# Kernel optimization log

Measured on AMD Instinct MI355X. Metric: run time of the kernel, lower is better.

## Reference

```python
import jax, jax.numpy as jnp
import numpy as np

B, N, E = 32, 256, 300   # batch, num hyperedges, word emb size
H, K = 256, 8            # nhidden, nhead
MARGIN = 0.2


def setup_inputs() -> dict:
    key = jax.random.key(0)
    ks = jax.random.split(key, 10)
    s_in = 1.0 / np.sqrt(E)
    s_h = 1.0 / np.sqrt(H)
    s_fc = 1.0 / np.sqrt(H * K)
    return {
        'he_anchor': jax.random.normal(ks[0], (B, N, E), jnp.float32),
        'he_pos': jax.random.normal(ks[1], (B, N, E), jnp.float32),
        'he_neg': jax.random.normal(ks[2], (B, N, E), jnp.float32),
        'W_a2h': jax.random.uniform(ks[3], (H, E), jnp.float32, -s_in, s_in),
        'b_a2h': jax.random.uniform(ks[4], (H,), jnp.float32, -s_in, s_in),
        'W_c2h': jax.random.uniform(ks[5], (H, E), jnp.float32, -s_in, s_in),
        'b_c2h': jax.random.uniform(ks[6], (H,), jnp.float32, -s_in, s_in),
        'W_att': jax.random.uniform(ks[7], (K, H), jnp.float32, -s_h, s_h),
        'b_att': jax.random.uniform(ks[8], (K,), jnp.float32, -s_h, s_h),
        'W_fc': jax.random.uniform(ks[9], (1, H * K), jnp.float32, -s_fc, s_fc),
        'b_fc': jnp.zeros((1,), jnp.float32),
    }


def _score(x, y, W_a2h, b_a2h, W_c2h, b_c2h, W_att, b_att, W_fc, b_fc):
    # a2h / c2h projections, then permute to [B, H, N]
    Aa = jnp.transpose(x @ W_a2h.T + b_a2h, (0, 2, 1))  # [B,H,N]
    Ac = jnp.transpose(y @ W_c2h.T + b_c2h, (0, 2, 1))  # [B,H,M]
    # h2att applied to the outer product Aa[b,h,n]*Ac[b,h,m]; fuse into one einsum
    logits = jnp.einsum('bhn,bhm,kh->bknm', Aa, Ac, W_att) + b_att[None, :, None, None]
    b_, k_, n_, m_ = logits.shape
    att = jax.nn.softmax(logits.reshape(b_, k_, n_ * m_), axis=-1).reshape(b_, k_, n_, m_)
    # per-head bilinear aggregation: out[b,k,h] = sum_{n,m} Aa[b,h,n]*att[b,k,n,m]*Ac[b,h,m]
    t = jnp.einsum('bhn,bknm->bkhm', Aa, att)
    out = jnp.einsum('bkhm,bhm->bkh', t, Ac)
    # torch concat order is head-major: [B, K*H]
    out = out.reshape(b_, k_ * H)
    return out @ W_fc.T + b_fc  # [B,1]


def reference(he_anchor, he_pos, he_neg, W_a2h, b_a2h, W_c2h, b_c2h, W_att, b_att, W_fc, b_fc):
    score_p = _score(he_anchor, he_pos, W_a2h, b_a2h, W_c2h, b_c2h, W_att, b_att, W_fc, b_fc)
    score_n = _score(he_anchor, he_neg, W_a2h, b_a2h, W_c2h, b_c2h, W_att, b_att, W_fc, b_fc)
    loss = jnp.mean(jax.nn.relu(score_n - score_p + MARGIN))
    return loss
```

## Files before the change

### kernel.cpp

```cpp
#include <hip/hip_runtime.h>

#define BB 32
#define NN 256
#define EE 300
#define HH 256
#define KK 8
#define MARGINF 0.2f
#define EP 320

typedef __attribute__((ext_vector_type(8))) short bf16x8;
typedef __attribute__((ext_vector_type(4))) float f32x4;
typedef __attribute__((ext_vector_type(16))) float f32x16;

__device__ inline ushort f2bf(float f) {
  unsigned u = __float_as_uint(f);
  u += 0x7fffu + ((u >> 16) & 1u);
  return (ushort)(u >> 16);
}
__device__ inline float bf2f(ushort s) { return __uint_as_float(((unsigned)s) << 16); }
__device__ inline unsigned cvtpk(float lo, float hi) {
  unsigned r;
  asm("v_cvt_pk_bf16_f32 %0, %1, %2" : "=v"(r) : "v"(lo), "v"(hi));
  return r;
}
__device__ inline void gload_lds16(const ushort* g, ushort* l) {
  __builtin_amdgcn_global_load_lds(
      (const __attribute__((address_space(1))) void*)g,
      (__attribute__((address_space(3))) void*)l, 16, 0, 0);
}

__global__ __launch_bounds__(256) void wconv_kernel(
    const float* __restrict__ Wa, const float* __restrict__ Wc,
    ushort* __restrict__ Wt, unsigned* __restrict__ counter)
{
  const int i = blockIdx.x * 256 + threadIdx.x;
  if (i == 0) counter[0] = 0u;
  const int w = i / 81920;
  int r = i - w * 81920;
  const int hb = r / 5120; r -= hb * 5120;
  const int ks = r / 512;  r -= ks * 512;
  const int l = r >> 3, j = r & 7;
  const int h = hb * 16 + (l & 15);
  const int e = ks * 32 + (l >> 4) * 8 + j;
  const float* src = w ? Wc : Wa;
  Wt[i] = (e < EE) ? f2bf(src[h * EE + e]) : (ushort)0;
}

__global__ __launch_bounds__(256, 3) void proj_kernel(
    const float* __restrict__ he_a, const float* __restrict__ he_p,
    const float* __restrict__ he_n, const ushort* __restrict__ Wt,
    const float* __restrict__ b_a2h, const float* __restrict__ b_c2h,
    ushort* __restrict__ AT)
{
  const int z = blockIdx.y;
  const int which = z >> 5;
  const int b = z & 31;
  const int nb = blockIdx.x;
  const int n0 = nb * 32;
  const int tid = threadIdx.x;
  const int wv = tid >> 6;
  const int lane = tid & 63;
  const int col = lane & 15;
  const int quad = lane >> 4;

  const float* X = (which == 0 ? he_a : which == 1 ? he_p : he_n) + (size_t)b * NN * EE;
  const ushort* W = Wt + (size_t)(which == 0 ? 0 : 1) * 81920;
  const float* bias = (which == 0 ? b_a2h : b_c2h);

  __shared__ __align__(16) ushort sX[32][328];
  __shared__ __align__(16) ushort tr[32][264];

  {
    const int row = tid >> 3, seg = tid & 7;
    const float* xr = X + (size_t)(n0 + row) * EE;
#pragma unroll
    for (int q = 0; q < 10; q++) {
      const int jj = seg + 8 * q;
      float4 xv = {0.f, 0.f, 0.f, 0.f};
      if (jj < 75) xv = *(const float4*)&xr[4 * jj];
      uint2 p; p.x = cvtpk(xv.x, xv.y); p.y = cvtpk(xv.z, xv.w);
      *(uint2*)&sX[row][4 * jj] = p;
    }
  }
  __syncthreads();

  f32x4 acc[2][4];
#pragma unroll
  for (int nf = 0; nf < 2; nf++)
#pragma unroll
    for (int mb = 0; mb < 4; mb++) acc[nf][mb] = (f32x4){0.f, 0.f, 0.f, 0.f};

#pragma unroll
  for (int ks = 0; ks < 10; ks++) {
    const int off = 32 * ks + 8 * quad;
    const bf16x8 a0 = *(const bf16x8*)&sX[col][off];
    const bf16x8 a1 = *(const bf16x8*)&sX[16 + col][off];
#pragma unroll
    for (int mb = 0; mb < 4; mb++) {
      const bf16x8 w8 = *(const bf16x8*)&W[(4 * wv + mb) * 5120 + ks * 512 + lane * 8];
      acc[0][mb] = __builtin_amdgcn_mfma_f32_16x16x32_bf16(a0, w8, acc[0][mb], 0, 0, 0);
      acc[1][mb] = __builtin_amdgcn_mfma_f32_16x16x32_bf16(a1, w8, acc[1][mb], 0, 0, 0);
    }
  }

#pragma unroll
  for (int nf = 0; nf < 2; nf++)
#pragma unroll
    for (int mb = 0; mb < 4; mb++) {
      const float bi = bias[64 * wv + 16 * mb + col];
#pragma unroll
      for (int r = 0; r < 4; r++)
        tr[16 * nf + 4 * quad + r][64 * wv + 16 * mb + col] = f2bf(acc[nf][mb][r] + bi);
    }
  __syncthreads();
  {
    ushort* dst = AT + (size_t)(which * BB + b) * (NN * HH) + (size_t)nb * 8192;
#pragma unroll
    for (int it = 0; it < 4; it++) {
      const int c = it * 256 + tid;
      const int row = c & 31, hs = (c >> 5) & 1, hb = c >> 6;
      *(uint4*)&dst[c * 8] = *(const uint4*)&tr[row][hb * 16 + hs * 8];
    }
  }
}

__global__ __launch_bounds__(256, 2) void attn_kernel(
    const ushort* __restrict__ AT, const float* __restrict__ Watt,
    const float* __restrict__ Wfc, const float* __restrict__ bfc,
    float* __restrict__ scoresK, unsigned* __restrict__ counter,
    float* __restrict__ out)
{
  const int d = blockIdx.x;
  const int x = d & 7;
  const int j = d >> 3;
  const int grp = x * 8 + (j & 7);
  const int k = j >> 3;
  const int which = grp >> 5;
  const int b = grp & 31;
  const int idx = k * 64 + grp;
  const int tid = threadIdx.x;
  const int wv = tid >> 6;
  const int lane = tid & 63;

  const ushort* Ta = AT + (size_t)b * (NN * HH);
  const ushort* Tc = AT + (size_t)((1 + which) * BB + b) * (NN * HH);

  __shared__ __align__(16) ushort sB[2][16384];
  __shared__ __align__(16) float wkf[256];
  __shared__ __align__(16) float wff[256];
  __shared__ float red[8];
  __shared__ unsigned isLast;

  wkf[tid] = Watt[(size_t)k * HH + tid];
  wff[tid] = Wfc[(size_t)k * HH + tid];
  __syncthreads();

  float num = 0.f, den = 0.f;

#pragma unroll 1
  for (int s = 0; s < 2; s++) {
#pragma unroll
    for (int it = 0; it < 8; it++) {
      const int off = it * 2048 + wv * 512;
      gload_lds16(Tc + off + lane * 8, &sB[0][off]);
    }

    const int nbk = 4 * s + wv;
    bf16x8 saf[16], gaf[16];
    const ushort* abase = Ta + nbk * 8192 + lane * 8;
#pragma unroll
    for (int ks = 0; ks < 16; ks++) {
      const bf16x8 a = *(const bf16x8*)&abase[ks * 512];
      const int off = 16 * ks + 8 * (lane >> 5);
      const float4 wa = *(const float4*)&wkf[off];
      const float4 wb = *(const float4*)&wkf[off + 4];
      const float4 fa = *(const float4*)&wff[off];
      const float4 fb = *(const float4*)&wff[off + 4];
      const float w[8] = {wa.x, wa.y, wa.z, wa.w, wb.x, wb.y, wb.z, wb.w};
      const float f[8] = {fa.x, fa.y, fa.z, fa.w, fb.x, fb.y, fb.z, fb.w};
      union { bf16x8 v; unsigned u[4]; } sv, gv;
#pragma unroll
      for (int jj = 0; jj < 4; jj++) {
        const float a0 = bf2f((ushort)a[2 * jj]), a1 = bf2f((ushort)a[2 * jj + 1]);
        sv.u[jj] = cvtpk(a0 * w[2 * jj], a1 * w[2 * jj + 1]);
        gv.u[jj] = cvtpk(a0 * f[2 * jj], a1 * f[2 * jj + 1]);
      }
      saf[ks] = sv.v; gaf[ks] = gv.v;
    }
    __syncthreads();

#pragma unroll 1
    for (int mc = 0; mc < 4; mc++) {
      const int cur = mc & 1;
      if (mc < 3) {
        const ushort* src = Tc + (mc + 1) * 16384;
#pragma unroll
        for (int it = 0; it < 8; it++) {
          const int off = it * 2048 + wv * 512;
          gload_lds16(src + off + lane * 8, &sB[cur ^ 1][off]);
        }
      }

      f32x16 aS0 = {0,0,0,0,0,0,0,0,0,0,0,0,0,0,0,0};
      f32x16 aS1 = {0,0,0,0,0,0,0,0,0,0,0,0,0,0,0,0};
      f32x16 aG0 = {0,0,0,0,0,0,0,0,0,0,0,0,0,0,0,0};
      f32x16 aG1 = {0,0,0,0,0,0,0,0,0,0,0,0,0,0,0,0};
#pragma unroll
      for (int ks = 0; ks < 16; ks++) {
        const bf16x8 b0 = *(const bf16x8*)&sB[cur][ks * 512 + lane * 8];
        const bf16x8 b1 = *(const bf16x8*)&sB[cur][8192 + ks * 512 + lane * 8];
        aS0 = __builtin_amdgcn_mfma_f32_32x32x16_bf16(saf[ks], b0, aS0, 0, 0, 0);
        aG0 = __builtin_amdgcn_mfma_f32_32x32x16_bf16(gaf[ks], b0, aG0, 0, 0, 0);
        aS1 = __builtin_amdgcn_mfma_f32_32x32x16_bf16(saf[ks], b1, aS1, 0, 0, 0);
        aG1 = __builtin_amdgcn_mfma_f32_32x32x16_bf16(gaf[ks], b1, aG1, 0, 0, 0);
      }
#pragma unroll
      for (int r = 0; r < 16; r++) {
        const float p0 = __expf(aS0[r]);
        den += p0; num += p0 * aG0[r];
        const float p1 = __expf(aS1[r]);
        den += p1; num += p1 * aG1[r];
      }
      __syncthreads();
    }
  }

#pragma unroll
  for (int off = 32; off >= 1; off >>= 1) {
    num += __shfl_xor(num, off);
    den += __shfl_xor(den, off);
  }
  if (lane == 0) { red[wv] = num; red[4 + wv] = den; }
  __syncthreads();
  if (tid == 0) {
    const float nt = red[0] + red[1] + red[2] + red[3];
    const float dt = red[4] + red[5] + red[6] + red[7];
    atomicExch(&scoresK[idx], nt / dt);
    __threadfence();
    isLast = (atomicAdd(counter, 1u) == 511u) ? 1u : 0u;
  }
  __syncthreads();

  if (isLast && tid < 64) {
    float s = bfc[0];
#pragma unroll
    for (int kk = 0; kk < KK; kk++)
      s += atomicAdd(&scoresK[kk * 64 + tid], 0.0f);
    const float other = __shfl(s, tid + 32);
    float v = 0.f;
    if (tid < 32) v = fmaxf(other - s + MARGINF, 0.f);
#pragma unroll
    for (int off = 32; off >= 1; off >>= 1) v += __shfl_xor(v, off);
    if (tid == 0) out[0] = v * (1.0f / 32.0f);
  }
}

extern "C" void kernel_launch(void* const* d_in, const int* in_sizes, int n_in,
                              void* d_out, int out_size, void* d_ws, size_t ws_size,
                              hipStream_t stream) {
  const float* he_a  = (const float*)d_in[0];
  const float* he_p  = (const float*)d_in[1];
  const float* he_n  = (const float*)d_in[2];
  const float* W_a2h = (const float*)d_in[3];
  const float* b_a2h = (const float*)d_in[4];
  const float* W_c2h = (const float*)d_in[5];
  const float* b_c2h = (const float*)d_in[6];
  const float* W_att = (const float*)d_in[7];
  const float* W_fc  = (const float*)d_in[9];
  const float* b_fc  = (const float*)d_in[10];

  ushort* AT = (ushort*)d_ws;
  float* scoresK = (float*)(AT + (size_t)3 * BB * NN * HH);
  ushort* Wt = (ushort*)(scoresK + 512);
  unsigned* counter = (unsigned*)(Wt + (size_t)2 * HH * EP);
  (void)ws_size; (void)in_sizes; (void)n_in; (void)out_size;

  wconv_kernel<<<640, 256, 0, stream>>>(W_a2h, W_c2h, Wt, counter);
  dim3 pg(8, 96);
  proj_kernel<<<pg, 256, 0, stream>>>(he_a, he_p, he_n, Wt, b_a2h, b_c2h, AT);
  attn_kernel<<<512, 256, 0, stream>>>(AT, W_att, W_fc, b_fc, scoresK, counter, (float*)d_out);
}
```

Baseline: 137.1 us.

## Split attention work across more, smaller blocks with atomic num/den accumulation

The attention kernel now runs 2048 blocks of 128 threads instead of 512 blocks of 256. Each block covers a quarter of the n-range (two n-blocks) and processes one 32-column m tile per step over 8 steps, with a smaller LDS double buffer. Partial softmax numerators and denominators are added atomically into a zero-initialised workspace, and the last block combines them. It also raises MFMA issue priority around the inner loop. The goal is better occupancy and load balance on the GPU, at the cost of re-reading the Tc tiles four times as often, more atomics, and less reuse of each B tile per wave.

```diff
diff --git a/kernel.cpp b/kernel.cpp
--- a/kernel.cpp
+++ b/kernel.cpp
@@ -31,10 +31,12 @@
 
 __global__ __launch_bounds__(256) void wconv_kernel(
     const float* __restrict__ Wa, const float* __restrict__ Wc,
-    ushort* __restrict__ Wt, unsigned* __restrict__ counter)
+    ushort* __restrict__ Wt, float* __restrict__ numden,
+    unsigned* __restrict__ counter)
 {
   const int i = blockIdx.x * 256 + threadIdx.x;
   if (i == 0) counter[0] = 0u;
+  if (i < 1024) numden[i] = 0.f;
   const int w = i / 81920;
   int r = i - w * 81920;
   const int hb = r / 5120; r -= hb * 5120;
@@ -124,17 +126,19 @@
   }
 }
 
-__global__ __launch_bounds__(256, 2) void attn_kernel(
+__global__ __launch_bounds__(128, 2) void attn_kernel(
     const ushort* __restrict__ AT, const float* __restrict__ Watt,
     const float* __restrict__ Wfc, const float* __restrict__ bfc,
-    float* __restrict__ scoresK, unsigned* __restrict__ counter,
+    float* __restrict__ numden, unsigned* __restrict__ counter,
     float* __restrict__ out)
 {
   const int d = blockIdx.x;
   const int x = d & 7;
   const int j = d >> 3;
   const int grp = x * 8 + (j & 7);
-  const int k = j >> 3;
+  const int rest = j >> 3;
+  const int k = rest & 7;
+  const int np = rest >> 3;
   const int which = grp >> 5;
   const int b = grp & 31;
   const int idx = k * 64 + grp;
@@ -145,28 +149,27 @@
   const ushort* Ta = AT + (size_t)b * (NN * HH);
   const ushort* Tc = AT + (size_t)((1 + which) * BB + b) * (NN * HH);
 
-  __shared__ __align__(16) ushort sB[2][16384];
+  __shared__ __align__(16) ushort sB[2][8192];
   __shared__ __align__(16) float wkf[256];
   __shared__ __align__(16) float wff[256];
-  __shared__ float red[8];
+  __shared__ float red[4];
   __shared__ unsigned isLast;
 
   wkf[tid] = Watt[(size_t)k * HH + tid];
+  wkf[tid + 128] = Watt[(size_t)k * HH + tid + 128];
   wff[tid] = Wfc[(size_t)k * HH + tid];
-  __syncthreads();
-
-  float num = 0.f, den = 0.f;
-
-#pragma unroll 1
-  for (int s = 0; s < 2; s++) {
-#pragma unroll
-    for (int it = 0; it < 8; it++) {
-      const int off = it * 2048 + wv * 512;
-      gload_lds16(Tc + off + lane * 8, &sB[0][off]);
-    }
-
-    const int nbk = 4 * s + wv;
-    bf16x8 saf[16], gaf[16];
+  wff[tid + 128] = Wfc[(size_t)k * HH + tid + 128];
+  __syncthreads();
+
+#pragma unroll
+  for (int it = 0; it < 8; it++) {
+    const int off = it * 1024 + wv * 512;
+    gload_lds16(Tc + off + lane * 8, &sB[0][off]);
+  }
+
+  const int nbk = 2 * np + wv;
+  bf16x8 saf[16], gaf[16];
+  {
     const ushort* abase = Ta + nbk * 8192 + lane * 8;
 #pragma unroll
     for (int ks = 0; ks < 16; ks++) {
@@ -187,42 +190,39 @@
       }
       saf[ks] = sv.v; gaf[ks] = gv.v;
     }
+  }
+  __syncthreads();
+
+  float num = 0.f, den = 0.f;
+
+#pragma unroll 1
+  for (int t = 0; t < 8; t++) {
+    const int cur = t & 1;
+    if (t < 7) {
+      const ushort* src = Tc + (t + 1) * 8192;
+#pragma unroll
+      for (int it = 0; it < 8; it++) {
+        const int off = it * 1024 + wv * 512;
+        gload_lds16(src + off + lane * 8, &sB[cur ^ 1][off]);
+      }
+    }
+
+    f32x16 aS = {0,0,0,0,0,0,0,0,0,0,0,0,0,0,0,0};
+    f32x16 aG = {0,0,0,0,0,0,0,0,0,0,0,0,0,0,0,0};
+    __builtin_amdgcn_s_setprio(1);
+#pragma unroll
+    for (int ks = 0; ks < 16; ks++) {
+      const bf16x8 b0 = *(const bf16x8*)&sB[cur][ks * 512 + lane * 8];
+      aS = __builtin_amdgcn_mfma_f32_32x32x16_bf16(saf[ks], b0, aS, 0, 0, 0);
+      aG = __builtin_amdgcn_mfma_f32_32x32x16_bf16(gaf[ks], b0, aG, 0, 0, 0);
+    }
+    __builtin_amdgcn_s_setprio(0);
+#pragma unroll
+    for (int r = 0; r < 16; r++) {
+      const float p = __expf(aS[r]);
+      den += p; num += p * aG[r];
+    }
     __syncthreads();
-
-#pragma unroll 1
-    for (int mc = 0; mc < 4; mc++) {
-      const int cur = mc & 1;
-      if (mc < 3) {
-        const ushort* src = Tc + (mc + 1) * 16384;
-#pragma unroll
-        for (int it = 0; it < 8; it++) {
-          const int off = it * 2048 + wv * 512;
-          gload_lds16(src + off + lane * 8, &sB[cur ^ 1][off]);
-        }
-      }
-
-      f32x16 aS0 = {0,0,0,0,0,0,0,0,0,0,0,0,0,0,0,0};
-      f32x16 aS1 = {0,0,0,0,0,0,0,0,0,0,0,0,0,0,0,0};
-      f32x16 aG0 = {0,0,0,0,0,0,0,0,0,0,0,0,0,0,0,0};
-      f32x16 aG1 = {0,0,0,0,0,0,0,0,0,0,0,0,0,0,0,0};
-#pragma unroll
-      for (int ks = 0; ks < 16; ks++) {
-        const bf16x8 b0 = *(const bf16x8*)&sB[cur][ks * 512 + lane * 8];
-        const bf16x8 b1 = *(const bf16x8*)&sB[cur][8192 + ks * 512 + lane * 8];
-        aS0 = __builtin_amdgcn_mfma_f32_32x32x16_bf16(saf[ks], b0, aS0, 0, 0, 0);
-        aG0 = __builtin_amdgcn_mfma_f32_32x32x16_bf16(gaf[ks], b0, aG0, 0, 0, 0);
-        aS1 = __builtin_amdgcn_mfma_f32_32x32x16_bf16(saf[ks], b1, aS1, 0, 0, 0);
-        aG1 = __builtin_amdgcn_mfma_f32_32x32x16_bf16(gaf[ks], b1, aG1, 0, 0, 0);
-      }
-#pragma unroll
-      for (int r = 0; r < 16; r++) {
-        const float p0 = __expf(aS0[r]);
-        den += p0; num += p0 * aG0[r];
-        const float p1 = __expf(aS1[r]);
-        den += p1; num += p1 * aG1[r];
-      }
-      __syncthreads();
-    }
   }
 
 #pragma unroll
@@ -230,22 +230,25 @@
     num += __shfl_xor(num, off);
     den += __shfl_xor(den, off);
   }
-  if (lane == 0) { red[wv] = num; red[4 + wv] = den; }
+  if (lane == 0) { red[wv] = num; red[2 + wv] = den; }
   __syncthreads();
   if (tid == 0) {
-    const float nt = red[0] + red[1] + red[2] + red[3];
-    const float dt = red[4] + red[5] + red[6] + red[7];
-    atomicExch(&scoresK[idx], nt / dt);
+    atomicAdd(&numden[2 * idx], red[0] + red[1]);
+    atomicAdd(&numden[2 * idx + 1], red[2] + red[3]);
     __threadfence();
-    isLast = (atomicAdd(counter, 1u) == 511u) ? 1u : 0u;
+    isLast = (atomicAdd(counter, 1u) == 2047u) ? 1u : 0u;
   }
   __syncthreads();
 
   if (isLast && tid < 64) {
     float s = bfc[0];
 #pragma unroll
-    for (int kk = 0; kk < KK; kk++)
-      s += atomicAdd(&scoresK[kk * 64 + tid], 0.0f);
+    for (int kk = 0; kk < KK; kk++) {
+      const int id2 = 2 * (kk * 64 + tid);
+      const float nt = atomicAdd(&numden[id2], 0.0f);
+      const float dt = atomicAdd(&numden[id2 + 1], 0.0f);
+      s += nt / dt;
+    }
     const float other = __shfl(s, tid + 32);
     float v = 0.f;
     if (tid < 32) v = fmaxf(other - s + MARGINF, 0.f);
@@ -270,13 +273,13 @@
   const float* b_fc  = (const float*)d_in[10];
 
   ushort* AT = (ushort*)d_ws;
-  float* scoresK = (float*)(AT + (size_t)3 * BB * NN * HH);
-  ushort* Wt = (ushort*)(scoresK + 512);
+  float* numden = (float*)(AT + (size_t)3 * BB * NN * HH);
+  ushort* Wt = (ushort*)(numden + 1024);
   unsigned* counter = (unsigned*)(Wt + (size_t)2 * HH * EP);
   (void)ws_size; (void)in_sizes; (void)n_in; (void)out_size;
 
-  wconv_kernel<<<640, 256, 0, stream>>>(W_a2h, W_c2h, Wt, counter);
+  wconv_kernel<<<640, 256, 0, stream>>>(W_a2h, W_c2h, Wt, numden, counter);
   dim3 pg(8, 96);
   proj_kernel<<<pg, 256, 0, stream>>>(he_a, he_p, he_n, Wt, b_a2h, b_c2h, AT);
-  attn_kernel<<<512, 256, 0, stream>>>(AT, W_att, W_fc, b_fc, scoresK, counter, (float*)d_out);
-}
+  attn_kernel<<<2048, 128, 0, stream>>>(AT, W_att, W_fc, b_fc, numden, counter, (float*)d_out);
+}
```

Result: slower. 164.6 us (+20.1%).

## Hold both anchor row-blocks in registers and stream each C chunk once

Applied to the files above, without the earlier changes.

Each wave now keeps the scaled anchor fragments for both of its n-blocks in registers and walks the four C chunks a single time, where it previously walked them twice. This halves the global-to-LDS traffic and barrier count for the C operand. In exchange, the launch bound drops to one block per SIMD pair to allow roughly double the fragment registers, which lowers occupancy. The change also raises wave priority around the MFMA loop and switches the accumulation to fmaf.

```diff
diff --git a/kernel.cpp b/kernel.cpp
--- a/kernel.cpp
+++ b/kernel.cpp
@@ -124,7 +124,7 @@
   }
 }
 
-__global__ __launch_bounds__(256, 2) void attn_kernel(
+__global__ __launch_bounds__(256, 1) void attn_kernel(
     const ushort* __restrict__ AT, const float* __restrict__ Watt,
     const float* __restrict__ Wfc, const float* __restrict__ bfc,
     float* __restrict__ scoresK, unsigned* __restrict__ counter,
@@ -155,19 +155,16 @@
   wff[tid] = Wfc[(size_t)k * HH + tid];
   __syncthreads();
 
-  float num = 0.f, den = 0.f;
-
-#pragma unroll 1
-  for (int s = 0; s < 2; s++) {
-#pragma unroll
-    for (int it = 0; it < 8; it++) {
-      const int off = it * 2048 + wv * 512;
-      gload_lds16(Tc + off + lane * 8, &sB[0][off]);
-    }
-
-    const int nbk = 4 * s + wv;
-    bf16x8 saf[16], gaf[16];
-    const ushort* abase = Ta + nbk * 8192 + lane * 8;
+#pragma unroll
+  for (int it = 0; it < 8; it++) {
+    const int off = it * 2048 + wv * 512;
+    gload_lds16(Tc + off + lane * 8, &sB[0][off]);
+  }
+
+  bf16x8 saf[2][16], gaf[2][16];
+#pragma unroll
+  for (int nn = 0; nn < 2; nn++) {
+    const ushort* abase = Ta + (4 * nn + wv) * 8192 + lane * 8;
 #pragma unroll
     for (int ks = 0; ks < 16; ks++) {
       const bf16x8 a = *(const bf16x8*)&abase[ks * 512];
@@ -185,44 +182,50 @@
         sv.u[jj] = cvtpk(a0 * w[2 * jj], a1 * w[2 * jj + 1]);
         gv.u[jj] = cvtpk(a0 * f[2 * jj], a1 * f[2 * jj + 1]);
       }
-      saf[ks] = sv.v; gaf[ks] = gv.v;
-    }
-    __syncthreads();
+      saf[nn][ks] = sv.v; gaf[nn][ks] = gv.v;
+    }
+  }
+  __syncthreads();
+
+  float num = 0.f, den = 0.f;
 
 #pragma unroll 1
-    for (int mc = 0; mc < 4; mc++) {
-      const int cur = mc & 1;
-      if (mc < 3) {
-        const ushort* src = Tc + (mc + 1) * 16384;
-#pragma unroll
-        for (int it = 0; it < 8; it++) {
-          const int off = it * 2048 + wv * 512;
-          gload_lds16(src + off + lane * 8, &sB[cur ^ 1][off]);
-        }
-      }
-
+  for (int mc = 0; mc < 4; mc++) {
+    const int cur = mc & 1;
+    if (mc < 3) {
+      const ushort* src = Tc + (mc + 1) * 16384;
+#pragma unroll
+      for (int it = 0; it < 8; it++) {
+        const int off = it * 2048 + wv * 512;
+        gload_lds16(src + off + lane * 8, &sB[cur ^ 1][off]);
+      }
+    }
+
+#pragma unroll
+    for (int mb = 0; mb < 2; mb++) {
       f32x16 aS0 = {0,0,0,0,0,0,0,0,0,0,0,0,0,0,0,0};
+      f32x16 aG0 = {0,0,0,0,0,0,0,0,0,0,0,0,0,0,0,0};
       f32x16 aS1 = {0,0,0,0,0,0,0,0,0,0,0,0,0,0,0,0};
-      f32x16 aG0 = {0,0,0,0,0,0,0,0,0,0,0,0,0,0,0,0};
       f32x16 aG1 = {0,0,0,0,0,0,0,0,0,0,0,0,0,0,0,0};
+      __builtin_amdgcn_s_setprio(1);
 #pragma unroll
       for (int ks = 0; ks < 16; ks++) {
-        const bf16x8 b0 = *(const bf16x8*)&sB[cur][ks * 512 + lane * 8];
-        const bf16x8 b1 = *(const bf16x8*)&sB[cur][8192 + ks * 512 + lane * 8];
-        aS0 = __builtin_amdgcn_mfma_f32_32x32x16_bf16(saf[ks], b0, aS0, 0, 0, 0);
-        aG0 = __builtin_amdgcn_mfma_f32_32x32x16_bf16(gaf[ks], b0, aG0, 0, 0, 0);
-        aS1 = __builtin_amdgcn_mfma_f32_32x32x16_bf16(saf[ks], b1, aS1, 0, 0, 0);
-        aG1 = __builtin_amdgcn_mfma_f32_32x32x16_bf16(gaf[ks], b1, aG1, 0, 0, 0);
-      }
+        const bf16x8 bf = *(const bf16x8*)&sB[cur][mb * 8192 + ks * 512 + lane * 8];
+        aS0 = __builtin_amdgcn_mfma_f32_32x32x16_bf16(saf[0][ks], bf, aS0, 0, 0, 0);
+        aG0 = __builtin_amdgcn_mfma_f32_32x32x16_bf16(gaf[0][ks], bf, aG0, 0, 0, 0);
+        aS1 = __builtin_amdgcn_mfma_f32_32x32x16_bf16(saf[1][ks], bf, aS1, 0, 0, 0);
+        aG1 = __builtin_amdgcn_mfma_f32_32x32x16_bf16(gaf[1][ks], bf, aG1, 0, 0, 0);
+      }
+      __builtin_amdgcn_s_setprio(0);
 #pragma unroll
       for (int r = 0; r < 16; r++) {
         const float p0 = __expf(aS0[r]);
-        den += p0; num += p0 * aG0[r];
+        den += p0; num = fmaf(p0, aG0[r], num);
         const float p1 = __expf(aS1[r]);
-        den += p1; num += p1 * aG1[r];
-      }
-      __syncthreads();
-    }
+        den += p1; num = fmaf(p1, aG1[r], num);
+      }
+    }
+    __syncthreads();
   }
 
 #pragma unroll
```

New measurement: 153.7 us. 1.12x slower.

## Share full Ac tile across two heads per 512-thread block in attn kernel

Applied to the files above, without the earlier changes.

Each attention block now has 512 threads and handles two heads for the same (which,b) pair. The whole 256x256 Ac tile is loaded into LDS once and shared by both heads, which halves Ac global traffic and removes the per-chunk double-buffer syncs. Waves rotate their starting chunk and their s order to spread out LDS access, and they raise MFMA priority with setprio. The head weights are now stored in LDS as bf16, a small precision change. The kernel uses 128KB of LDS and occupancy drops to one block per CU with half the grid, which risks less latency hiding.

```diff
diff --git a/kernel.cpp b/kernel.cpp
--- a/kernel.cpp
+++ b/kernel.cpp
@@ -124,7 +124,7 @@
   }
 }
 
-__global__ __launch_bounds__(256, 2) void attn_kernel(
+__global__ __launch_bounds__(512, 1) void attn_kernel(
     const ushort* __restrict__ AT, const float* __restrict__ Watt,
     const float* __restrict__ Wfc, const float* __restrict__ bfc,
     float* __restrict__ scoresK, unsigned* __restrict__ counter,
@@ -134,94 +134,92 @@
   const int x = d & 7;
   const int j = d >> 3;
   const int grp = x * 8 + (j & 7);
-  const int k = j >> 3;
+  const int kp = j >> 3;
   const int which = grp >> 5;
   const int b = grp & 31;
-  const int idx = k * 64 + grp;
   const int tid = threadIdx.x;
-  const int wv = tid >> 6;
+  const int wid = tid >> 6;
+  const int kh = wid >> 2;
+  const int ws = wid & 3;
   const int lane = tid & 63;
+  const int k = 2 * kp + kh;
 
   const ushort* Ta = AT + (size_t)b * (NN * HH);
   const ushort* Tc = AT + (size_t)((1 + which) * BB + b) * (NN * HH);
 
-  __shared__ __align__(16) ushort sB[2][16384];
-  __shared__ __align__(16) float wkf[256];
-  __shared__ __align__(16) float wff[256];
-  __shared__ float red[8];
+  __shared__ __align__(16) ushort sB[65536];
+  __shared__ __align__(16) ushort wkb[2][256];
+  __shared__ __align__(16) ushort wfb[2][256];
+  __shared__ float red[16];
   __shared__ unsigned isLast;
 
-  wkf[tid] = Watt[(size_t)k * HH + tid];
-  wff[tid] = Wfc[(size_t)k * HH + tid];
-  __syncthreads();
+#pragma unroll
+  for (int it = 0; it < 16; it++) {
+    const int off = (wid * 16 + it) * 512;
+    gload_lds16(Tc + off + lane * 8, &sB[off]);
+  }
+  {
+    const int h = tid & 255, hd = tid >> 8;
+    const int kt = 2 * kp + hd;
+    wkb[hd][h] = f2bf(Watt[(size_t)kt * HH + h]);
+    wfb[hd][h] = f2bf(Wfc[(size_t)kt * HH + h]);
+  }
+  __syncthreads();
+
+  const ushort* wkp = wkb[kh];
+  const ushort* wfp = wfb[kh];
 
   float num = 0.f, den = 0.f;
 
 #pragma unroll 1
-  for (int s = 0; s < 2; s++) {
-#pragma unroll
-    for (int it = 0; it < 8; it++) {
-      const int off = it * 2048 + wv * 512;
-      gload_lds16(Tc + off + lane * 8, &sB[0][off]);
-    }
-
-    const int nbk = 4 * s + wv;
+  for (int si = 0; si < 2; si++) {
+    const int s = si ^ kh;
     bf16x8 saf[16], gaf[16];
-    const ushort* abase = Ta + nbk * 8192 + lane * 8;
-#pragma unroll
-    for (int ks = 0; ks < 16; ks++) {
-      const bf16x8 a = *(const bf16x8*)&abase[ks * 512];
-      const int off = 16 * ks + 8 * (lane >> 5);
-      const float4 wa = *(const float4*)&wkf[off];
-      const float4 wb = *(const float4*)&wkf[off + 4];
-      const float4 fa = *(const float4*)&wff[off];
-      const float4 fb = *(const float4*)&wff[off + 4];
-      const float w[8] = {wa.x, wa.y, wa.z, wa.w, wb.x, wb.y, wb.z, wb.w};
-      const float f[8] = {fa.x, fa.y, fa.z, fa.w, fb.x, fb.y, fb.z, fb.w};
-      union { bf16x8 v; unsigned u[4]; } sv, gv;
-#pragma unroll
-      for (int jj = 0; jj < 4; jj++) {
-        const float a0 = bf2f((ushort)a[2 * jj]), a1 = bf2f((ushort)a[2 * jj + 1]);
-        sv.u[jj] = cvtpk(a0 * w[2 * jj], a1 * w[2 * jj + 1]);
-        gv.u[jj] = cvtpk(a0 * f[2 * jj], a1 * f[2 * jj + 1]);
+    {
+      const ushort* abase = Ta + (4 * s + ws) * 8192 + lane * 8;
+#pragma unroll
+      for (int ks = 0; ks < 16; ks++) {
+        const bf16x8 a = *(const bf16x8*)&abase[ks * 512];
+        const int off = 16 * ks + 8 * (lane >> 5);
+        const bf16x8 w8 = *(const bf16x8*)&wkp[off];
+        const bf16x8 f8 = *(const bf16x8*)&wfp[off];
+        union { bf16x8 v; unsigned u[4]; } sv, gv;
+#pragma unroll
+        for (int jj = 0; jj < 4; jj++) {
+          const float a0 = bf2f((ushort)a[2 * jj]), a1 = bf2f((ushort)a[2 * jj + 1]);
+          sv.u[jj] = cvtpk(a0 * bf2f((ushort)w8[2 * jj]), a1 * bf2f((ushort)w8[2 * jj + 1]));
+          gv.u[jj] = cvtpk(a0 * bf2f((ushort)f8[2 * jj]), a1 * bf2f((ushort)f8[2 * jj + 1]));
+        }
+        saf[ks] = sv.v; gaf[ks] = gv.v;
       }
-      saf[ks] = sv.v; gaf[ks] = gv.v;
-    }
-    __syncthreads();
+    }
 
 #pragma unroll 1
-    for (int mc = 0; mc < 4; mc++) {
-      const int cur = mc & 1;
-      if (mc < 3) {
-        const ushort* src = Tc + (mc + 1) * 16384;
-#pragma unroll
-        for (int it = 0; it < 8; it++) {
-          const int off = it * 2048 + wv * 512;
-          gload_lds16(src + off + lane * 8, &sB[cur ^ 1][off]);
-        }
-      }
-
+    for (int mi = 0; mi < 4; mi++) {
+      const int mtp = (mi + ws) & 3;
+      const int mbase = mtp * 16384;
       f32x16 aS0 = {0,0,0,0,0,0,0,0,0,0,0,0,0,0,0,0};
+      f32x16 aG0 = {0,0,0,0,0,0,0,0,0,0,0,0,0,0,0,0};
       f32x16 aS1 = {0,0,0,0,0,0,0,0,0,0,0,0,0,0,0,0};
-      f32x16 aG0 = {0,0,0,0,0,0,0,0,0,0,0,0,0,0,0,0};
       f32x16 aG1 = {0,0,0,0,0,0,0,0,0,0,0,0,0,0,0,0};
+      __builtin_amdgcn_s_setprio(1);
 #pragma unroll
       for (int ks = 0; ks < 16; ks++) {
-        const bf16x8 b0 = *(const bf16x8*)&sB[cur][ks * 512 + lane * 8];
-        const bf16x8 b1 = *(const bf16x8*)&sB[cur][8192 + ks * 512 + lane * 8];
+        const bf16x8 b0 = *(const bf16x8*)&sB[mbase + ks * 512 + lane * 8];
+        const bf16x8 b1 = *(const bf16x8*)&sB[mbase + 8192 + ks * 512 + lane * 8];
         aS0 = __builtin_amdgcn_mfma_f32_32x32x16_bf16(saf[ks], b0, aS0, 0, 0, 0);
         aG0 = __builtin_amdgcn_mfma_f32_32x32x16_bf16(gaf[ks], b0, aG0, 0, 0, 0);
         aS1 = __builtin_amdgcn_mfma_f32_32x32x16_bf16(saf[ks], b1, aS1, 0, 0, 0);
         aG1 = __builtin_amdgcn_mfma_f32_32x32x16_bf16(gaf[ks], b1, aG1, 0, 0, 0);
       }
+      __builtin_amdgcn_s_setprio(0);
 #pragma unroll
       for (int r = 0; r < 16; r++) {
         const float p0 = __expf(aS0[r]);
-        den += p0; num += p0 * aG0[r];
+        den += p0; num = fmaf(p0, aG0[r], num);
         const float p1 = __expf(aS1[r]);
-        den += p1; num += p1 * aG1[r];
+        den += p1; num = fmaf(p1, aG1[r], num);
       }
-      __syncthreads();
     }
   }
 
@@ -230,14 +228,17 @@
     num += __shfl_xor(num, off);
     den += __shfl_xor(den, off);
   }
-  if (lane == 0) { red[wv] = num; red[4 + wv] = den; }
+  if (lane == 0) { red[wid] = num; red[8 + wid] = den; }
   __syncthreads();
   if (tid == 0) {
-    const float nt = red[0] + red[1] + red[2] + red[3];
-    const float dt = red[4] + red[5] + red[6] + red[7];
-    atomicExch(&scoresK[idx], nt / dt);
+    const float n0 = red[0] + red[1] + red[2] + red[3];
+    const float d0 = red[8] + red[9] + red[10] + red[11];
+    const float n1 = red[4] + red[5] + red[6] + red[7];
+    const float d1 = red[12] + red[13] + red[14] + red[15];
+    atomicExch(&scoresK[(2 * kp) * 64 + grp], n0 / d0);
+    atomicExch(&scoresK[(2 * kp + 1) * 64 + grp], n1 / d1);
     __threadfence();
-    isLast = (atomicAdd(counter, 1u) == 511u) ? 1u : 0u;
+    isLast = (atomicAdd(counter, 1u) == 255u) ? 1u : 0u;
   }
   __syncthreads();
 
@@ -278,5 +279,5 @@
   wconv_kernel<<<640, 256, 0, stream>>>(W_a2h, W_c2h, Wt, counter);
   dim3 pg(8, 96);
   proj_kernel<<<pg, 256, 0, stream>>>(he_a, he_p, he_n, Wt, b_a2h, b_c2h, AT);
-  attn_kernel<<<512, 256, 0, stream>>>(AT, W_att, W_fc, b_fc, scoresK, counter, (float*)d_out);
-}
+  attn_kernel<<<256, 512, 0, stream>>>(AT, W_att, W_fc, b_fc, scoresK, counter, (float*)d_out);
+}
```

New measurement: 132.5 us. -3.3%, faster.
